# Performance work log

Hardware: AMD Instinct MI355X
Metric: run time of the kernel (lower is better)

The kernel has to match this reference:

```python
import jax, jax.numpy as jnp
import numpy as np
import math

B, L, D, H, FF = 8, 4096, 1024, 16, 4
BELOW, ABOVE = 1, 1
DH = D // H


def _timing_signal(length, channels, min_ts=1.0, max_ts=10000.0):
    position = np.arange(length)
    num_timescales = channels // 2
    log_inc = math.log(max_ts / min_ts) / (num_timescales - 1)
    inv = min_ts * np.exp(np.arange(num_timescales).astype(float) * -log_inc)
    scaled = position[:, None] * inv[None, :]
    sig = np.zeros((length, channels))
    sig[:, 0::2] = np.sin(scaled)
    sig[:, 1::2] = np.cos(scaled)
    return jnp.asarray(sig[None], dtype=jnp.float32)  # [1, L, D]


def setup_inputs() -> dict:
    key = jax.random.key(0)
    ks = jax.random.split(key, 8)
    s = lambda k, sh: jax.random.normal(k, sh, jnp.float32) * 0.02
    return dict(
        X=jax.random.normal(ks[0], (B, L, D), jnp.float32),
        src_mask=jnp.zeros((B, L), jnp.bool_),  # True = padding
        pe=_timing_signal(L, D),
        Wq=s(ks[1], (D, D)), Wk=s(ks[2], (D, D)), Wv=s(ks[3], (D, D)),
        bq=jnp.zeros((D,), jnp.float32), bk=jnp.zeros((D,), jnp.float32), bv=jnp.zeros((D,), jnp.float32),
        Wo=s(ks[4], (D, D)), bo=jnp.zeros((D,), jnp.float32),
        g1=jnp.ones((D,), jnp.float32), beta1=jnp.zeros((D,), jnp.float32),
        W1=s(ks[5], (D, FF * D)), b1=jnp.zeros((FF * D,), jnp.float32),
        W2=s(ks[6], (FF * D, D)), b2=jnp.zeros((D,), jnp.float32),
        g2=jnp.ones((D,), jnp.float32), beta2=jnp.zeros((D,), jnp.float32),
    )


def _layernorm(x, g, b, eps=1e-5):
    m = x.mean(-1, keepdims=True)
    v = ((x - m) ** 2).mean(-1, keepdims=True)
    return (x - m) * jax.lax.rsqrt(v + eps) * g + b


def reference(X, src_mask, pe, Wq, Wk, Wv, bq, bk, bv, Wo, bo,
              g1, beta1, W1, b1, W2, b2, g2, beta2):
    # positional encoding (dropout is identity in eval)
    X = X + pe  # [B, L, D]

    # QKV projections -> [B, L, H, DH]
    q = (X @ Wq + bq).reshape(B, L, H, DH)
    k = (X @ Wk + bk).reshape(B, L, H, DH)
    v = (X @ Wv + bv).reshape(B, L, H, DH)

    # Banded (diagonal-window) attention: query i attends keys i-BELOW..i+ABOVE.
    Wwin = BELOW + ABOVE + 1
    idx = jnp.arange(L)[:, None] + jnp.arange(-BELOW, ABOVE + 1)[None, :]  # [L, Wwin]
    valid = (idx >= 0) & (idx < L)
    idxc = jnp.clip(idx, 0, L - 1)
    kw = k[:, idxc]  # [B, L, Wwin, H, DH]
    vw = v[:, idxc]

    scores = jnp.einsum('blhd,blwhd->bhlw', q, kw) / jnp.sqrt(jnp.float32(DH))
    key_ok = ~src_mask  # [B, L]
    allow = valid[None, :, :] & key_ok[:, idxc]  # [B, L, Wwin]
    scores = jnp.where(allow[:, None, :, :], scores, jnp.float32(-1e30))
    attn = jax.nn.softmax(scores, axis=-1)  # [B, H, L, Wwin]
    ctx = jnp.einsum('bhlw,blwhd->blhd', attn, vw).reshape(B, L, D)
    Xt = ctx @ Wo + bo

    # post-norm residual blocks (dropout identity in eval)
    X = _layernorm(X + Xt, g1, beta1)
    ffn = jnp.maximum(X @ W1 + b1, 0.0) @ W2 + b2
    X = _layernorm(X + ffn, g2, beta2)
    return X
```

## Files before the change

kernel.cpp:

```cpp
#include <hip/hip_runtime.h>
#include <hip/hip_bf16.h>

#define B_  8
#define L_  4096
#define D_  1024
#define H_  16
#define MTOT (B_*L_)
#define NFF  (4*D_)
#define CH   4096

typedef __bf16 bf16_t;
typedef float  f32x4 __attribute__((ext_vector_type(4)));
typedef __bf16 b16x8 __attribute__((ext_vector_type(8)));
typedef __bf16 b16x4 __attribute__((ext_vector_type(4)));

#define OFF_WQKVT ((size_t)0)
#define OFF_WOT   ((size_t)6291456)
#define OFF_W1T   ((size_t)8388608)
#define OFF_W2T   ((size_t)16777216)
#define OFF_BQKV  ((size_t)25165824)
#define OFF_XB    ((size_t)33554432)
#define OFF_B     ((size_t)100663296)

__global__ __launch_bounds__(256) void k_add_pe(const float* __restrict__ X,
                                                const float* __restrict__ pe,
                                                bf16_t* __restrict__ Xb)
{
    size_t i  = ((size_t)blockIdx.x * 256 + threadIdx.x) * 4;
    size_t ld = i & ((size_t)L_ * D_ - 1);
    float4 x = *(const float4*)(X + i);
    float4 p = *(const float4*)(pe + ld);
    b16x4 b;
    b[0] = (bf16_t)(x.x + p.x); b[1] = (bf16_t)(x.y + p.y);
    b[2] = (bf16_t)(x.z + p.z); b[3] = (bf16_t)(x.w + p.w);
    *(b16x4*)(Xb + i) = b;
}

__global__ __launch_bounds__(256) void k_prep(const float* __restrict__ Wq,
                                              const float* __restrict__ Wk,
                                              const float* __restrict__ Wv,
                                              const float* __restrict__ Wo,
                                              const float* __restrict__ W1,
                                              const float* __restrict__ W2,
                                              const float* __restrict__ bq,
                                              const float* __restrict__ bk,
                                              const float* __restrict__ bv,
                                              bf16_t* __restrict__ WqkvT,
                                              bf16_t* __restrict__ WoT,
                                              bf16_t* __restrict__ W1T,
                                              bf16_t* __restrict__ W2T,
                                              float* __restrict__ bqkv)
{
    const int id = blockIdx.x;
    if (id >= 12288) {
        const int i = (id - 12288) * 256 + threadIdx.x;
        if (i < 1024)       bqkv[i] = bq[i];
        else if (i < 2048)  bqkv[i] = bk[i - 1024];
        else if (i < 3072)  bqkv[i] = bv[i - 2048];
        return;
    }
    const float* src; bf16_t* dst; int K, N, t;
    if (id < 4096) {
        const int w = id >> 10; t = id & 1023; K = 1024; N = 1024;
        src = (w == 0) ? Wq : (w == 1) ? Wk : (w == 2) ? Wv : Wo;
        dst = (w < 3) ? (WqkvT + (size_t)w * 1024 * 1024) : WoT;
    } else if (id < 8192) {
        t = id - 4096; K = 1024; N = 4096; src = W1; dst = W1T;
    } else {
        t = id - 8192; K = 4096; N = 1024; src = W2; dst = W2T;
    }
    const int ntiles = N >> 5;
    const int n0 = (t % ntiles) << 5;
    const int k0 = (t / ntiles) << 5;

    __shared__ float tt[32][33];
    const int tx = threadIdx.x & 31;
    const int ty = threadIdx.x >> 5;
    #pragma unroll
    for (int i = ty; i < 32; i += 8)
        tt[i][tx] = src[(size_t)(k0 + i) * N + n0 + tx];
    __syncthreads();
    #pragma unroll
    for (int i = ty; i < 32; i += 8)
        dst[(size_t)(n0 + i) * K + k0 + tx] = (bf16_t)tt[tx][i];
}

#define BM 128
#define BN 128
#define BK 32

__device__ __forceinline__ void gload_lds16(const void* g, char* lds_byte) {
    __builtin_amdgcn_global_load_lds((const __attribute__((address_space(1))) void*)g,
                                     (__attribute__((address_space(3))) void*)lds_byte,
                                     16, 0, 0);
}

template<int EPI>
__global__ __launch_bounds__(256, 4) void k_gemm_bt(const bf16_t* __restrict__ A,
                                                    const bf16_t* __restrict__ Bt,
                                                    const float* __restrict__ bias,
                                                    void* __restrict__ Cv,
                                                    const int N, const int K)
{
    __shared__ __align__(16) bf16_t As[BM * BK];
    __shared__ __align__(16) bf16_t Bs[BN * BK];
    const int tid  = threadIdx.x;
    const int wave = tid >> 6;
    const int lane = tid & 63;

    const int Nt = gridDim.x, Mt = gridDim.y;
    const int lid = blockIdx.y * Nt + blockIdx.x;
    int bm, bn;
    {
        const int xcd = lid & 7;
        const int s   = lid >> 3;
        bm = xcd * (Mt >> 3) + s / Nt;
        bn = s % Nt;
    }
    const int n0 = bn * BN;
    const int m0 = bm * BM;
    const int waveM = wave >> 1;
    const int waveN = wave & 1;

    const int srow = tid >> 2;
    const int scol = (tid & 3) << 3;
    const bf16_t* ag  = A  + (size_t)(m0 + srow)      * K + scol;
    const bf16_t* ag2 = A  + (size_t)(m0 + 64 + srow) * K + scol;
    const bf16_t* bg  = Bt + (size_t)(n0 + srow)      * K + scol;
    const bf16_t* bg2 = Bt + (size_t)(n0 + 64 + srow) * K + scol;

    char* ldsA = (char*)&As[0] + wave * 1024;
    char* ldsB = (char*)&Bs[0] + wave * 1024;

    const bf16_t* AsP = As + (waveM * 64 + (lane & 15)) * BK + ((lane >> 4) << 3);
    const bf16_t* BsP = Bs + (waveN * 64 + (lane & 15)) * BK + ((lane >> 4) << 3);

    f32x4 acc[4][4] = {};

    for (int kt = 0; kt < K; kt += BK) {
        __syncthreads();
        gload_lds16(ag,  ldsA);
        gload_lds16(ag2, ldsA + 4096);
        gload_lds16(bg,  ldsB);
        gload_lds16(bg2, ldsB + 4096);
        ag += BK; ag2 += BK; bg += BK; bg2 += BK;
        __syncthreads();
        b16x8 af[4], bfr[4];
        #pragma unroll
        for (int i = 0; i < 4; ++i) af[i]  = *(const b16x8*)(AsP + i * 16 * BK);
        #pragma unroll
        for (int i = 0; i < 4; ++i) bfr[i] = *(const b16x8*)(BsP + i * 16 * BK);
        #pragma unroll
        for (int mi = 0; mi < 4; ++mi)
            #pragma unroll
            for (int ni = 0; ni < 4; ++ni)
                acc[mi][ni] = __builtin_amdgcn_mfma_f32_16x16x32_bf16(af[mi], bfr[ni], acc[mi][ni], 0, 0, 0);
    }

    const int rbase = m0 + waveM * 64 + ((lane >> 4) << 2);
    const int cbase = n0 + waveN * 64 + (lane & 15);
    #pragma unroll
    for (int mi = 0; mi < 4; ++mi) {
        #pragma unroll
        for (int ni = 0; ni < 4; ++ni) {
            const int col = cbase + ni * 16;
            const float bb = bias[col];
            #pragma unroll
            for (int r = 0; r < 4; ++r) {
                const int rowg = rbase + mi * 16 + r;
                float v = acc[mi][ni][r] + bb;
                if (EPI == 2) v = fmaxf(v, 0.0f);
                if (EPI == 0) ((float*)Cv)[(size_t)rowg * N + col] = v;
                else          ((bf16_t*)Cv)[(size_t)rowg * N + col] = (bf16_t)v;
            }
        }
    }
}

__global__ __launch_bounds__(256) void k_attn(const bf16_t* __restrict__ QKV,
                                              const unsigned char* __restrict__ mask,
                                              bf16_t* __restrict__ ctx)
{
    const int wid  = (blockIdx.x << 2) + (threadIdx.x >> 6);
    const int lane = threadIdx.x & 63;
    const int h    = wid & (H_ - 1);
    const int l    = wid >> 4;

    const float q = (float)QKV[(size_t)l * 3072 + h * 64 + lane];
    float sc[3], vv[3];
    bool  ok[3];
    #pragma unroll
    for (int w = 0; w < 3; ++w) {
        const int lw  = l + w - 1;
        const bool valid = (unsigned)lw < (unsigned)L_;
        const int lwc = lw < 0 ? 0 : (lw > L_ - 1 ? L_ - 1 : lw);
        const size_t rb = (size_t)lwc * 3072 + h * 64 + lane;
        const float kk = (float)QKV[rb + 1024];
        vv[w] = (float)QKV[rb + 2048];
        ok[w] = valid && (mask[lwc] == 0);
        sc[w] = q * kk;
    }
    #pragma unroll
    for (int off = 32; off; off >>= 1) {
        sc[0] += __shfl_xor(sc[0], off);
        sc[1] += __shfl_xor(sc[1], off);
        sc[2] += __shfl_xor(sc[2], off);
    }
    const float s0 = ok[0] ? sc[0] * 0.125f : -1e30f;
    const float s1 = ok[1] ? sc[1] * 0.125f : -1e30f;
    const float s2 = ok[2] ? sc[2] * 0.125f : -1e30f;
    const float mx = fmaxf(s0, fmaxf(s1, s2));
    const float e0 = __expf(s0 - mx), e1 = __expf(s1 - mx), e2 = __expf(s2 - mx);
    const float inv = 1.0f / (e0 + e1 + e2);
    const float o = (e0 * vv[0] + e1 * vv[1] + e2 * vv[2]) * inv;
    ctx[(size_t)l * 1024 + h * 64 + lane] = (bf16_t)o;
}

template<int FINAL>
__global__ __launch_bounds__(256) void k_res_ln(const bf16_t* __restrict__ Xres,
                                                const float* __restrict__ Y,
                                                const float* __restrict__ g,
                                                const float* __restrict__ beta,
                                                bf16_t* __restrict__ outB,
                                                float* __restrict__ outF)
{
    const int row = blockIdx.x;
    const int tid = threadIdx.x;
    const size_t base = (size_t)row * D_ + tid * 4;
    b16x4  xr = *(const b16x4*)(Xres + base);
    float4 y  = *(const float4*)(Y + base);
    const float t0 = (float)xr[0] + y.x, t1 = (float)xr[1] + y.y;
    const float t2 = (float)xr[2] + y.z, t3 = (float)xr[3] + y.w;
    float s = t0 + t1 + t2 + t3;
    float q = t0*t0 + t1*t1 + t2*t2 + t3*t3;
    #pragma unroll
    for (int off = 32; off; off >>= 1) {
        s += __shfl_xor(s, off);
        q += __shfl_xor(q, off);
    }
    __shared__ float red[8];
    const int wv = tid >> 6, ln = tid & 63;
    if (ln == 0) { red[wv] = s; red[wv + 4] = q; }
    __syncthreads();
    s = red[0] + red[1] + red[2] + red[3];
    q = red[4] + red[5] + red[6] + red[7];
    const float mean = s * (1.0f / D_);
    const float var  = q * (1.0f / D_) - mean * mean;
    const float rs   = rsqrtf(var + 1e-5f);
    const int c = tid * 4;
    float4 gv = *(const float4*)(g + c);
    float4 bv = *(const float4*)(beta + c);
    float o0 = (t0 - mean) * rs * gv.x + bv.x;
    float o1 = (t1 - mean) * rs * gv.y + bv.y;
    float o2 = (t2 - mean) * rs * gv.z + bv.z;
    float o3 = (t3 - mean) * rs * gv.w + bv.w;
    if (FINAL) {
        float4 o; o.x = o0; o.y = o1; o.z = o2; o.w = o3;
        *(float4*)(outF + base) = o;
    } else {
        b16x4 b; b[0] = (bf16_t)o0; b[1] = (bf16_t)o1; b[2] = (bf16_t)o2; b[3] = (bf16_t)o3;
        *(b16x4*)(outB + base) = b;
    }
}

extern "C" void kernel_launch(void* const* d_in, const int* in_sizes, int n_in,
                              void* d_out, int out_size, void* d_ws, size_t ws_size,
                              hipStream_t stream)
{
    const float* X    = (const float*)d_in[0];
    const unsigned char* mask = (const unsigned char*)d_in[1];
    const float* pe   = (const float*)d_in[2];
    const float* Wq   = (const float*)d_in[3];
    const float* Wk   = (const float*)d_in[4];
    const float* Wv   = (const float*)d_in[5];
    const float* bq   = (const float*)d_in[6];
    const float* bk   = (const float*)d_in[7];
    const float* bv   = (const float*)d_in[8];
    const float* Wo   = (const float*)d_in[9];
    const float* bo   = (const float*)d_in[10];
    const float* g1   = (const float*)d_in[11];
    const float* be1  = (const float*)d_in[12];
    const float* W1   = (const float*)d_in[13];
    const float* b1   = (const float*)d_in[14];
    const float* W2   = (const float*)d_in[15];
    const float* b2   = (const float*)d_in[16];
    const float* g2   = (const float*)d_in[17];
    const float* be2  = (const float*)d_in[18];

    char* ws = (char*)d_ws;
    bf16_t* WqkvT = (bf16_t*)(ws + OFF_WQKVT);
    bf16_t* WoT   = (bf16_t*)(ws + OFF_WOT);
    bf16_t* W1T   = (bf16_t*)(ws + OFF_W1T);
    bf16_t* W2T   = (bf16_t*)(ws + OFF_W2T);
    float*  bqkv  = (float*) (ws + OFF_BQKV);
    bf16_t* Xb    = (bf16_t*)(ws + OFF_XB);
    float*  Y     = (float*)d_out;

    const bool big = ws_size >= (size_t)234881024;

    k_add_pe<<<MTOT * D_ / 1024, 256, 0, stream>>>(X, pe, Xb);

    k_prep<<<12300, 256, 0, stream>>>(Wq, Wk, Wv, Wo, W1, W2, bq, bk, bv,
                                      WqkvT, WoT, W1T, W2T, bqkv);

    if (big) {
        bf16_t* ctx  = (bf16_t*)(ws + OFF_B);
        bf16_t* qkvc = (bf16_t*)(ws + OFF_B + 67108864);
        for (int b = 0; b < B_; ++b) {
            k_gemm_bt<1><<<dim3(3072/BN, CH/BM), 256, 0, stream>>>(
                Xb + (size_t)b*CH*D_, WqkvT, bqkv, qkvc, 3072, 1024);
            k_attn<<<CH*H_/4, 256, 0, stream>>>(qkvc, mask + (size_t)b*CH,
                                                ctx + (size_t)b*CH*D_);
        }
        k_gemm_bt<0><<<dim3(1024/BN, MTOT/BM), 256, 0, stream>>>(ctx, WoT, bo, Y, 1024, 1024);
        k_res_ln<0><<<MTOT, 256, 0, stream>>>(Xb, Y, g1, be1, Xb, nullptr);
        bf16_t* hb = (bf16_t*)(ws + OFF_B);
        for (int c = 0; c < 2; ++c) {
            const size_t r0 = (size_t)c * 16384;
            k_gemm_bt<2><<<dim3(NFF/BN, 16384/BM), 256, 0, stream>>>(
                Xb + r0*D_, W1T, b1, hb, NFF, 1024);
            k_gemm_bt<0><<<dim3(1024/BN, 16384/BM), 256, 0, stream>>>(
                hb, W2T, b2, Y + r0*D_, 1024, NFF);
        }
        k_res_ln<1><<<MTOT, 256, 0, stream>>>(Xb, Y, g2, be2, nullptr, (float*)d_out);
    } else {
        bf16_t* qkvc = (bf16_t*)(ws + OFF_B);
        bf16_t* ctxc = (bf16_t*)(ws + OFF_B + 25165824);
        for (int b = 0; b < B_; ++b) {
            const size_t r0 = (size_t)b * CH;
            k_gemm_bt<1><<<dim3(3072/BN, CH/BM), 256, 0, stream>>>(
                Xb + r0*D_, WqkvT, bqkv, qkvc, 3072, 1024);
            k_attn<<<CH*H_/4, 256, 0, stream>>>(qkvc, mask + r0, ctxc);
            k_gemm_bt<0><<<dim3(1024/BN, CH/BM), 256, 0, stream>>>(
                ctxc, WoT, bo, Y + r0*D_, 1024, 1024);
        }
        k_res_ln<0><<<MTOT, 256, 0, stream>>>(Xb, Y, g1, be1, Xb, nullptr);
        bf16_t* hb = (bf16_t*)(ws + OFF_B);
        for (int c = 0; c < 8; ++c) {
            const size_t r0 = (size_t)c * CH;
            k_gemm_bt<2><<<dim3(NFF/BN, CH/BM), 256, 0, stream>>>(
                Xb + r0*D_, W1T, b1, hb, NFF, 1024);
            k_gemm_bt<0><<<dim3(1024/BN, CH/BM), 256, 0, stream>>>(
                hb, W2T, b2, Y + r0*D_, 1024, NFF);
        }
        k_res_ln<1><<<MTOT, 256, 0, stream>>>(Xb, Y, g2, be2, nullptr, (float*)d_out);
    }
}
```

Before: 1.547 ms.

## Double GEMM K-tile with XOR-swizzled LDS and chunk QKV/attention over two batches

```diff
diff --git a/kernel.cpp b/kernel.cpp
--- a/kernel.cpp
+++ b/kernel.cpp
@@ -7,7 +7,6 @@
 #define H_  16
 #define MTOT (B_*L_)
 #define NFF  (4*D_)
-#define CH   4096
 
 typedef __bf16 bf16_t;
 typedef float  f32x4 __attribute__((ext_vector_type(4)));
@@ -87,7 +86,7 @@
 
 #define BM 128
 #define BN 128
-#define BK 32
+#define BK 64
 
 __device__ __forceinline__ void gload_lds16(const void* g, char* lds_byte) {
     __builtin_amdgcn_global_load_lds((const __attribute__((address_space(1))) void*)g,
@@ -122,34 +121,46 @@
     const int waveM = wave >> 1;
     const int waveN = wave & 1;
 
-    const int srow = tid >> 2;
-    const int scol = (tid & 3) << 3;
-    const bf16_t* ag  = A  + (size_t)(m0 + srow)      * K + scol;
-    const bf16_t* ag2 = A  + (size_t)(m0 + 64 + srow) * K + scol;
-    const bf16_t* bg  = Bt + (size_t)(n0 + srow)      * K + scol;
-    const bf16_t* bg2 = Bt + (size_t)(n0 + 64 + srow) * K + scol;
-
+    const int srow   = tid >> 3;
+    const int schunk = (tid & 7) ^ (srow & 7);
+    const bf16_t* ag = A  + (size_t)(m0 + srow) * K + schunk * 8;
+    const bf16_t* bg = Bt + (size_t)(n0 + srow) * K + schunk * 8;
+    const size_t rstep = (size_t)32 * K;
     char* ldsA = (char*)&As[0] + wave * 1024;
     char* ldsB = (char*)&Bs[0] + wave * 1024;
 
-    const bf16_t* AsP = As + (waveM * 64 + (lane & 15)) * BK + ((lane >> 4) << 3);
-    const bf16_t* BsP = Bs + (waveN * 64 + (lane & 15)) * BK + ((lane >> 4) << 3);
+    const int q   = lane >> 4;
+    const int x7  = lane & 7;
+    const int sl0 = ((q)     ^ x7) << 3;
+    const int sl1 = ((4 + q) ^ x7) << 3;
+    const bf16_t* AsP = As + (waveM * 64 + (lane & 15)) * BK;
+    const bf16_t* BsP = Bs + (waveN * 64 + (lane & 15)) * BK;
 
     f32x4 acc[4][4] = {};
 
     for (int kt = 0; kt < K; kt += BK) {
         __syncthreads();
-        gload_lds16(ag,  ldsA);
-        gload_lds16(ag2, ldsA + 4096);
-        gload_lds16(bg,  ldsB);
-        gload_lds16(bg2, ldsB + 4096);
-        ag += BK; ag2 += BK; bg += BK; bg2 += BK;
+        #pragma unroll
+        for (int c = 0; c < 4; ++c) {
+            gload_lds16(ag + c * rstep, ldsA + c * 4096);
+            gload_lds16(bg + c * rstep, ldsB + c * 4096);
+        }
+        ag += BK; bg += BK;
         __syncthreads();
         b16x8 af[4], bfr[4];
         #pragma unroll
-        for (int i = 0; i < 4; ++i) af[i]  = *(const b16x8*)(AsP + i * 16 * BK);
-        #pragma unroll
-        for (int i = 0; i < 4; ++i) bfr[i] = *(const b16x8*)(BsP + i * 16 * BK);
+        for (int i = 0; i < 4; ++i) af[i]  = *(const b16x8*)(AsP + i * 16 * BK + sl0);
+        #pragma unroll
+        for (int i = 0; i < 4; ++i) bfr[i] = *(const b16x8*)(BsP + i * 16 * BK + sl0);
+        #pragma unroll
+        for (int mi = 0; mi < 4; ++mi)
+            #pragma unroll
+            for (int ni = 0; ni < 4; ++ni)
+                acc[mi][ni] = __builtin_amdgcn_mfma_f32_16x16x32_bf16(af[mi], bfr[ni], acc[mi][ni], 0, 0, 0);
+        #pragma unroll
+        for (int i = 0; i < 4; ++i) af[i]  = *(const b16x8*)(AsP + i * 16 * BK + sl1);
+        #pragma unroll
+        for (int i = 0; i < 4; ++i) bfr[i] = *(const b16x8*)(BsP + i * 16 * BK + sl1);
         #pragma unroll
         for (int mi = 0; mi < 4; ++mi)
             #pragma unroll
@@ -185,20 +196,21 @@
     const int lane = threadIdx.x & 63;
     const int h    = wid & (H_ - 1);
     const int l    = wid >> 4;
-
-    const float q = (float)QKV[(size_t)l * 3072 + h * 64 + lane];
+    const int lb   = l & (L_ - 1);
+
+    const float qv = (float)QKV[(size_t)l * 3072 + h * 64 + lane];
     float sc[3], vv[3];
     bool  ok[3];
     #pragma unroll
     for (int w = 0; w < 3; ++w) {
-        const int lw  = l + w - 1;
-        const bool valid = (unsigned)lw < (unsigned)L_;
-        const int lwc = lw < 0 ? 0 : (lw > L_ - 1 ? L_ - 1 : lw);
-        const size_t rb = (size_t)lwc * 3072 + h * 64 + lane;
+        const int d   = w - 1;
+        const bool valid = (unsigned)(lb + d) < (unsigned)L_;
+        const int dc  = valid ? d : 0;
+        const size_t rb = (size_t)(l + dc) * 3072 + h * 64 + lane;
         const float kk = (float)QKV[rb + 1024];
         vv[w] = (float)QKV[rb + 2048];
-        ok[w] = valid && (mask[lwc] == 0);
-        sc[w] = q * kk;
+        ok[w] = valid && (mask[l + dc] == 0);
+        sc[w] = qv * kk;
     }
     #pragma unroll
     for (int off = 32; off; off >>= 1) {
@@ -306,11 +318,11 @@
     if (big) {
         bf16_t* ctx  = (bf16_t*)(ws + OFF_B);
         bf16_t* qkvc = (bf16_t*)(ws + OFF_B + 67108864);
-        for (int b = 0; b < B_; ++b) {
-            k_gemm_bt<1><<<dim3(3072/BN, CH/BM), 256, 0, stream>>>(
-                Xb + (size_t)b*CH*D_, WqkvT, bqkv, qkvc, 3072, 1024);
-            k_attn<<<CH*H_/4, 256, 0, stream>>>(qkvc, mask + (size_t)b*CH,
-                                                ctx + (size_t)b*CH*D_);
+        for (int c = 0; c < 4; ++c) {
+            const size_t r0 = (size_t)c * 8192;
+            k_gemm_bt<1><<<dim3(3072/BN, 8192/BM), 256, 0, stream>>>(
+                Xb + r0*D_, WqkvT, bqkv, qkvc, 3072, 1024);
+            k_attn<<<8192*H_/4, 256, 0, stream>>>(qkvc, mask + r0, ctx + r0*D_);
         }
         k_gemm_bt<0><<<dim3(1024/BN, MTOT/BM), 256, 0, stream>>>(ctx, WoT, bo, Y, 1024, 1024);
         k_res_ln<0><<<MTOT, 256, 0, stream>>>(Xb, Y, g1, be1, Xb, nullptr);
@@ -327,20 +339,20 @@
         bf16_t* qkvc = (bf16_t*)(ws + OFF_B);
         bf16_t* ctxc = (bf16_t*)(ws + OFF_B + 25165824);
         for (int b = 0; b < B_; ++b) {
-            const size_t r0 = (size_t)b * CH;
-            k_gemm_bt<1><<<dim3(3072/BN, CH/BM), 256, 0, stream>>>(
+            const size_t r0 = (size_t)b * L_;
+            k_gemm_bt<1><<<dim3(3072/BN, L_/BM), 256, 0, stream>>>(
                 Xb + r0*D_, WqkvT, bqkv, qkvc, 3072, 1024);
-            k_attn<<<CH*H_/4, 256, 0, stream>>>(qkvc, mask + r0, ctxc);
-            k_gemm_bt<0><<<dim3(1024/BN, CH/BM), 256, 0, stream>>>(
+            k_attn<<<L_*H_/4, 256, 0, stream>>>(qkvc, mask + r0, ctxc);
+            k_gemm_bt<0><<<dim3(1024/BN, L_/BM), 256, 0, stream>>>(
                 ctxc, WoT, bo, Y + r0*D_, 1024, 1024);
         }
         k_res_ln<0><<<MTOT, 256, 0, stream>>>(Xb, Y, g1, be1, Xb, nullptr);
         bf16_t* hb = (bf16_t*)(ws + OFF_B);
         for (int c = 0; c < 8; ++c) {
-            const size_t r0 = (size_t)c * CH;
-            k_gemm_bt<2><<<dim3(NFF/BN, CH/BM), 256, 0, stream>>>(
+            const size_t r0 = (size_t)c * L_;
+            k_gemm_bt<2><<<dim3(NFF/BN, L_/BM), 256, 0, stream>>>(
                 Xb + r0*D_, W1T, b1, hb, NFF, 1024);
-            k_gemm_bt<0><<<dim3(1024/BN, CH/BM), 256, 0, stream>>>(
+            k_gemm_bt<0><<<dim3(1024/BN, L_/BM), 256, 0, stream>>>(
                 hb, W2T, b2, Y + r0*D_, 1024, NFF);
         }
         k_res_ln<1><<<MTOT, 256, 0, stream>>>(Xb, Y, g2, be2, nullptr, (float*)d_out);
```

After: 1.383 ms. 1.12x faster.
